# Kernel tuning notes

Hardware: AMD Instinct MI355X
Metric: run time of the kernel (lower is better)

The kernel has to match this reference:

```python
import jax, jax.numpy as jnp
import numpy as np

B, T, V = 8, 2048, 4096
BEAM = 8      # beam_size
BLANK = 0     # blank_id=0 in CTCBeamDecoder
TMP = 1.0     # temperature self.tmp


def setup_inputs() -> dict:
    key = jax.random.key(0)
    k1, k2 = jax.random.split(key)
    logits = jax.random.normal(k1, (B, T, V), dtype=jnp.float32)
    # valid frame counts in [T//2, T]
    lengths = jax.random.randint(k2, (B,), T // 2, T + 1).astype(jnp.int32)
    return {"logits": logits, "lengths": lengths}


def _beam_search_single(logP, length):
    """CTC beam search over alignments (no LM) for one utterance.
    logP: [T, V] log-probs, length: scalar valid frame count.
    Returns (collapsed_tokens [T] padded with -1, out_len, best_score).
    """
    scores0, toks0 = jax.lax.top_k(logP[0], BEAM)              # [BEAM]
    toks0 = toks0.astype(jnp.int32)
    bp0 = jnp.zeros((BEAM,), jnp.int32)

    def step(scores, xs):
        t, logp_t = xs
        cand = scores[:, None] + logp_t[None, :]               # [BEAM, V]
        new_scores, flat_idx = jax.lax.top_k(cand.reshape(-1), BEAM)
        bp = (flat_idx // V).astype(jnp.int32)
        tok = (flat_idx % V).astype(jnp.int32)
        valid = t < length
        new_scores = jnp.where(valid, new_scores, scores)
        bp = jnp.where(valid, bp, jnp.arange(BEAM, dtype=jnp.int32))
        tok = jnp.where(valid, tok, jnp.full((BEAM,), BLANK, jnp.int32))
        return new_scores, (tok, bp)

    ts = jnp.arange(1, T)
    final_scores, (toks, bps) = jax.lax.scan(step, scores0, (ts, logP[1:]))
    toks = jnp.concatenate([toks0[None], toks], axis=0)        # [T, BEAM]
    bps = jnp.concatenate([bp0[None], bps], axis=0)            # [T, BEAM]

    # backtrace best beam (index 0 after final top_k)
    def back(beam, xs):
        tok_t, bp_t = xs
        return bp_t[beam], tok_t[beam]
    _, path = jax.lax.scan(back, jnp.int32(0), (toks, bps), reverse=True)  # [T] in time order

    # CTC collapse: drop blanks and consecutive repeats, restrict to valid frames
    tpos = jnp.arange(T)
    prev = jnp.concatenate([jnp.array([-1], jnp.int32), path[:-1]])
    keep = (path != BLANK) & (path != prev) & (tpos < length)
    out_len = keep.sum().astype(jnp.int32)
    pos = jnp.cumsum(keep) - 1                                  # target slot for kept tokens
    idx = jnp.where(keep, pos, T)                               # dump non-kept into slot T
    out = jnp.full((T + 1,), -1, jnp.int32).at[idx].set(jnp.where(keep, path, -1))
    return out[:T], out_len, final_scores[0]


def reference(logits, lengths):
    # logits/tmp then log_softmax (the tensorized part of the torch module)
    logP = jax.nn.log_softmax(logits / TMP, axis=-1)            # [B, T, V]
    tokens, out_lens, best_scores = jax.vmap(_beam_search_single)(logP, lengths)
    return tokens, out_lens, best_scores, logP
```

## Files before the change

kernel.cpp:

```cpp
#include <hip/hip_runtime.h>
#include <cmath>

#define NB 8
#define NT 2048
#define NV 4096
#define NK 12

__device__ __forceinline__ void lds_fence() {
  asm volatile("s_waitcnt lgkmcnt(0)" ::: "memory");
}

__global__ __launch_bounds__(64, 4) void lsm_top12_kernel(
    const float* __restrict__ logits,
    float* __restrict__ out_logP,
    float* __restrict__ topPf,
    int* __restrict__ topI)
{
  const int row  = blockIdx.x;
  const int lane = threadIdx.x;
  const float4* __restrict__ x4 = (const float4*)(logits + (size_t)row * NV);

  float4 r[16];
  #pragma unroll
  for (int k = 0; k < 16; ++k) r[k] = x4[lane + (k << 6)];

  float m = -INFINITY;
  #pragma unroll
  for (int k = 0; k < 16; ++k)
    m = fmaxf(m, fmaxf(fmaxf(r[k].x, r[k].y), fmaxf(r[k].z, r[k].w)));
  #pragma unroll
  for (int off = 32; off > 0; off >>= 1) m = fmaxf(m, __shfl_xor(m, off, 64));

  float a0 = 0.0f, a1 = 0.0f, a2 = 0.0f, a3 = 0.0f;
  #pragma unroll
  for (int k = 0; k < 16; ++k) {
    a0 += __expf(r[k].x - m);
    a1 += __expf(r[k].y - m);
    a2 += __expf(r[k].z - m);
    a3 += __expf(r[k].w - m);
  }
  float accf = (a0 + a1) + (a2 + a3);
  #pragma unroll
  for (int off = 32; off > 0; off >>= 1) accf += __shfl_xor(accf, off, 64);
  const float L32 = logf(accf);

  float lv[NK]; int li[NK];
  #pragma unroll
  for (int z = 0; z < NK; ++z) { lv[z] = -INFINITY; li[z] = 0x7FFFFFFF; }

#define INS(VAL, IDX)                                                       \
  do {                                                                      \
    float _v = (VAL); int _i = (IDX);                                       \
    if (_v > lv[NK - 1]) {                                                  \
      lv[NK - 1] = _v; li[NK - 1] = _i;                                     \
      for (int z = NK - 1; z > 0; --z)                                      \
        if (lv[z] > lv[z - 1]) {                                            \
          float tv = lv[z]; lv[z] = lv[z - 1]; lv[z - 1] = tv;              \
          int   ti = li[z]; li[z] = li[z - 1]; li[z - 1] = ti;              \
        }                                                                   \
    }                                                                       \
  } while (0)

  float4* __restrict__ orow4 = (float4*)(out_logP + (size_t)row * NV);
  #pragma unroll
  for (int k = 0; k < 16; ++k) {
    const int vb = (lane + (k << 6)) << 2;
    float4 o;
    o.x = (r[k].x - m) - L32;
    o.y = (r[k].y - m) - L32;
    o.z = (r[k].z - m) - L32;
    o.w = (r[k].w - m) - L32;
    orow4[lane + (k << 6)] = o;
    const float g4 = fmaxf(fmaxf(o.x, o.y), fmaxf(o.z, o.w));
    if (g4 > lv[NK - 1]) {
      INS(o.x, vb); INS(o.y, vb + 1); INS(o.z, vb + 2); INS(o.w, vb + 3);
    }
  }
#undef INS

  float mv = 0.0f; int mi = 0;
  #pragma unroll
  for (int rr = 0; rr < NK; ++rr) {
    float cv = lv[0]; int ci = li[0];
    #pragma unroll
    for (int off = 32; off > 0; off >>= 1) {
      float ov = __shfl_xor(cv, off, 64);
      int   oi = __shfl_xor(ci, off, 64);
      if (ov > cv || (ov == cv && oi < ci)) { cv = ov; ci = oi; }
    }
    if (rr == 0)    { mv = cv; mi = ci; }
    if (lane == rr) { mv = cv; mi = ci; }
    if (lv[0] == cv && li[0] == ci) {
      for (int z = 0; z < NK - 1; ++z) { lv[z] = lv[z + 1]; li[z] = li[z + 1]; }
      lv[NK - 1] = -INFINITY; li[NK - 1] = 0x7FFFFFFF;
    }
  }
  if (lane < NK) {
    topPf[(size_t)row * NK + lane] = mv;
    topI [(size_t)row * NK + lane] = mi;
  }
}


#define LOADROW(P, V, R)                                                      \
  do {                                                                        \
    const int _r = (R) < NT ? (R) : (NT - 1);                                 \
    P = Pb[(size_t)_r * NK + j_l];                                            \
    V = Ib[(size_t)_r * NK + j_l];                                            \
  } while (0)

#define STEP(T, PV, VV)                                                       \
  do {                                                                        \
    const float cand = s + (PV);              \
    const unsigned int cb = ~__float_as_uint(cand);                           \
    const unsigned int flat = (unsigned int)((i_l << 12) | (VV));             \
    const unsigned long long key =                                            \
        ((unsigned long long)cb << 15) | (unsigned long long)(0x7FFFu ^ flat);\
    const unsigned int klo = (unsigned int)key;                               \
    const unsigned int khi = (unsigned int)(key >> 32);                       \
    int rank = 0;                                                             \
    _Pragma("unroll")                                                         \
    for (int mm = 0; mm < 31; ++mm) {                                         \
      const unsigned int olo =                                                \
          (unsigned int)__builtin_amdgcn_readlane((int)klo, mm);              \
      const unsigned int ohi =                                                \
          (unsigned int)__builtin_amdgcn_readlane((int)khi, mm);              \
      const unsigned long long ok = ((unsigned long long)ohi << 32) | olo;    \
      rank += (ok > key) ? 1 : 0;                                             \
    }                                                                         \
    const bool win = active && (rank < 8);                                    \
    const int sloti = win ? ((T) * 8 + rank) : (NT * 8 + lane);               \
    tokbp[sloti] = (unsigned short)(((VV) << 3) | i_l);                       \
    const int dst4 = win ? (rank << 2) : park4;                               \
    const int pushed =                                                        \
        __builtin_amdgcn_ds_permute(dst4, __float_as_int(cand));              \
    const float w0 = __uint_as_float((unsigned)__builtin_amdgcn_readlane(pushed, 0)); \
    const float w1 = __uint_as_float((unsigned)__builtin_amdgcn_readlane(pushed, 1)); \
    const float w2 = __uint_as_float((unsigned)__builtin_amdgcn_readlane(pushed, 2)); \
    const float w3 = __uint_as_float((unsigned)__builtin_amdgcn_readlane(pushed, 3)); \
    const float w4 = __uint_as_float((unsigned)__builtin_amdgcn_readlane(pushed, 4)); \
    const float w5 = __uint_as_float((unsigned)__builtin_amdgcn_readlane(pushed, 5)); \
    const float w6 = __uint_as_float((unsigned)__builtin_amdgcn_readlane(pushed, 6)); \
    const float w7 = __uint_as_float((unsigned)__builtin_amdgcn_readlane(pushed, 7)); \
    const float sA_ = b0 ? w1 : w0;                                           \
    const float sB_ = b0 ? w3 : w2;                                           \
    const float sC_ = b0 ? w5 : w4;                                           \
    const float sD_ = b0 ? w7 : w6;                                           \
    const float sE_ = b1 ? sB_ : sA_;                                         \
    const float sF_ = b1 ? sD_ : sC_;                                         \
    s = b2 ? sF_ : sE_;                                                       \
  } while (0)

__global__ __launch_bounds__(64) void beam_kernel(
    const float* __restrict__ topPf,
    const int* __restrict__ topI,
    const int* __restrict__ lengths,
    float* __restrict__ out_tok,
    float* __restrict__ out_lenA,
    float* __restrict__ out_scr)
{
  const int b    = blockIdx.x;
  const int lane = threadIdx.x;

  __shared__ unsigned short tokbp[NT * 8 + 64];
  __shared__ unsigned short pathA[NT];

  int len = lengths[b];
  if (len < 1) len = 1;
  if (len > NT) len = NT;

  int i_l = 0, j_l = 0; bool active = false;
  {
    int c = 0;
    #pragma unroll
    for (int i = 0; i < 8; ++i) {
      const int cnt = 12 / (i + 1);
      if (lane >= c && lane < c + cnt) { i_l = i; j_l = lane - c; active = true; }
      c += cnt;
    }
  }
  const bool b0 = (i_l & 1) != 0;
  const bool b1 = (i_l & 2) != 0;
  const bool b2 = (i_l & 4) != 0;
  const int  park4 = (32 + (lane & 31)) << 2;

  const float* __restrict__ Pb = topPf + (size_t)b * NT * NK;
  const int*   __restrict__ Ib = topI  + (size_t)b * NT * NK;

  {
    const float4* __restrict__ gp = (const float4*)Pb;
    const int4*   __restrict__ gi = (const int4*)Ib;
    float fa = 0.0f; int ia = 0;
    #pragma unroll 4
    for (int q = lane; q < NT * NK / 4; q += 64) {
      const float4 v = gp[q]; const int4 w = gi[q];
      fa += (v.x + v.y) + (v.z + v.w);
      ia ^= (w.x ^ w.y) ^ (w.z ^ w.w);
    }
    asm volatile("" :: "v"(fa), "v"(ia));
  }

  float s = Pb[i_l];
  if (lane < 8) tokbp[lane] = (unsigned short)(Ib[lane] << 3);

  float pA0, pA1, pA2, pA3, pB0, pB1, pB2, pB3;
  int   vA0, vA1, vA2, vA3, vB0, vB1, vB2, vB3;
  LOADROW(pA0, vA0, 1); LOADROW(pA1, vA1, 2);
  LOADROW(pA2, vA2, 3); LOADROW(pA3, vA3, 4);
  LOADROW(pB0, vB0, 5); LOADROW(pB1, vB1, 6);
  LOADROW(pB2, vB2, 7); LOADROW(pB3, vB3, 8);

  int t = 1;
  for (; t + 7 < len; t += 8) {
    STEP(t,     pA0, vA0);
    STEP(t + 1, pA1, vA1);
    STEP(t + 2, pA2, vA2);
    STEP(t + 3, pA3, vA3);
    LOADROW(pA0, vA0, t + 8);  LOADROW(pA1, vA1, t + 9);
    LOADROW(pA2, vA2, t + 10); LOADROW(pA3, vA3, t + 11);
    STEP(t + 4, pB0, vB0);
    STEP(t + 5, pB1, vB1);
    STEP(t + 6, pB2, vB2);
    STEP(t + 7, pB3, vB3);
    LOADROW(pB0, vB0, t + 12); LOADROW(pB1, vB1, t + 13);
    LOADROW(pB2, vB2, t + 14); LOADROW(pB3, vB3, t + 15);
  }
  if (t     < len) STEP(t,     pA0, vA0);
  if (t + 1 < len) STEP(t + 1, pA1, vA1);
  if (t + 2 < len) STEP(t + 2, pA2, vA2);
  if (t + 3 < len) STEP(t + 3, pA3, vA3);
  if (t + 4 < len) STEP(t + 4, pB0, vB0);
  if (t + 5 < len) STEP(t + 5, pB1, vB1);
  if (t + 6 < len) STEP(t + 6, pB2, vB2);

  lds_fence();
  if (lane == 0) {
    const uint4* __restrict__ rows = (const uint4*)tokbp;
#define EXT(R)                                                                \
    do {                                                                      \
      const unsigned long long half = (beam < 4)                              \
          ? (((unsigned long long)(R).y << 32) | (R).x)                       \
          : (((unsigned long long)(R).w << 32) | (R).z);                      \
      const int e = (int)((half >> ((beam & 3) << 4)) & 0xFFFFu);             \
      pathA[bt] = (unsigned short)(e >> 3);                                   \
      beam = e & 7;                                                           \
      --bt;                                                                   \
    } while (0)
    int beam = 0;
    int bt = len - 1;
    uint4 r0 = rows[bt];
    uint4 r1 = rows[bt >= 1 ? bt - 1 : 0];
    uint4 r2 = rows[bt >= 2 ? bt - 2 : 0];
    uint4 r3 = rows[bt >= 3 ? bt - 3 : 0];
    while (bt >= 7) {
      const uint4 n0 = rows[bt - 4], n1 = rows[bt - 5];
      const uint4 n2 = rows[bt - 6], n3 = rows[bt - 7];
      EXT(r0); EXT(r1); EXT(r2); EXT(r3);
      r0 = n0; r1 = n1; r2 = n2; r3 = n3;
    }
    while (bt >= 0) { const uint4 rr = rows[bt]; EXT(rr); }
#undef EXT
  }
  lds_fence();

  const int CH = NT / 64;
  const int base = lane * CH;
  int cnt = 0;
  for (int k = 0; k < CH; ++k) {
    int tt = base + k;
    if (tt < len) {
      int pt = pathA[tt];
      int pv = (tt > 0) ? (int)pathA[tt - 1] : -1;
      cnt += ((pt != 0) && (pt != pv)) ? 1 : 0;
    }
  }
  int incl = cnt;
  #pragma unroll
  for (int off = 1; off < 64; off <<= 1) {
    int n = __shfl_up(incl, off, 64);
    if (lane >= off) incl += n;
  }
  const int excl  = incl - cnt;
  const int total = __shfl(incl, 63, 64);

  float* __restrict__ ob = out_tok + (size_t)b * NT;
  int pos = excl;
  for (int k = 0; k < CH; ++k) {
    int tt = base + k;
    if (tt < len) {
      int pt = pathA[tt];
      int pv = (tt > 0) ? (int)pathA[tt - 1] : -1;
      if ((pt != 0) && (pt != pv)) { ob[pos] = (float)pt; ++pos; }
    }
  }
  for (int q = total + lane; q < NT; q += 64) ob[q] = -1.0f;

  if (lane == 0) {
    out_lenA[b] = (float)total;
    out_scr[b]  = s;
  }
}

#undef STEP
#undef LOADROW

extern "C" void kernel_launch(void* const* d_in, const int* in_sizes, int n_in,
                              void* d_out, int out_size, void* d_ws, size_t ws_size,
                              hipStream_t stream) {
  (void)in_sizes; (void)n_in; (void)out_size; (void)ws_size;
  const float* logits  = (const float*)d_in[0];
  const int*   lengths = (const int*)d_in[1];

  float* out_tok  = (float*)d_out;
  float* out_lenp = out_tok + NB * NT;
  float* out_scr  = out_lenp + NB;
  float* out_logP = out_scr + NB;

  float* topPf = (float*)d_ws;
  int*   topI  = (int*)(topPf + (size_t)NB * NT * NK);

  lsm_top12_kernel<<<NB * NT, 64, 0, stream>>>(logits, out_logP, topPf, topI);
  beam_kernel<<<NB, 64, 0, stream>>>(topPf, topI, lengths, out_tok, out_lenp, out_scr);
}
```

Measured before the change: 1.334 ms.

## Stream logsoftmax in chunks, split rank compare chains, drop cache prewarm

```diff
diff --git a/kernel.cpp b/kernel.cpp
--- a/kernel.cpp
+++ b/kernel.cpp
@@ -10,7 +10,7 @@
   asm volatile("s_waitcnt lgkmcnt(0)" ::: "memory");
 }
 
-__global__ __launch_bounds__(64, 4) void lsm_top12_kernel(
+__global__ __launch_bounds__(64, 6) void lsm_top12_kernel(
     const float* __restrict__ logits,
     float* __restrict__ out_logP,
     float* __restrict__ topPf,
@@ -20,26 +20,39 @@
   const int lane = threadIdx.x;
   const float4* __restrict__ x4 = (const float4*)(logits + (size_t)row * NV);
 
-  float4 r[16];
-  #pragma unroll
-  for (int k = 0; k < 16; ++k) r[k] = x4[lane + (k << 6)];
-
   float m = -INFINITY;
-  #pragma unroll
-  for (int k = 0; k < 16; ++k)
-    m = fmaxf(m, fmaxf(fmaxf(r[k].x, r[k].y), fmaxf(r[k].z, r[k].w)));
-  #pragma unroll
-  for (int off = 32; off > 0; off >>= 1) m = fmaxf(m, __shfl_xor(m, off, 64));
-
   float a0 = 0.0f, a1 = 0.0f, a2 = 0.0f, a3 = 0.0f;
-  #pragma unroll
-  for (int k = 0; k < 16; ++k) {
-    a0 += __expf(r[k].x - m);
-    a1 += __expf(r[k].y - m);
-    a2 += __expf(r[k].z - m);
-    a3 += __expf(r[k].w - m);
-  }
-  float accf = (a0 + a1) + (a2 + a3);
+  float4 f0 = x4[lane], f1 = x4[lane + 64], f2 = x4[lane + 128],
+         f3 = x4[lane + 192];
+  #pragma unroll
+  for (int c = 0; c < 4; ++c) {
+    float4 g0, g1, g2, g3;
+    if (c < 3) {
+      const int kb = lane + ((c + 1) << 8);
+      g0 = x4[kb]; g1 = x4[kb + 64]; g2 = x4[kb + 128]; g3 = x4[kb + 192];
+    } else { g0 = f0; g1 = f1; g2 = f2; g3 = f3; }
+    float cm = fmaxf(fmaxf(fmaxf(f0.x, f0.y), fmaxf(f0.z, f0.w)),
+                     fmaxf(fmaxf(f1.x, f1.y), fmaxf(f1.z, f1.w)));
+    cm = fmaxf(cm, fmaxf(fmaxf(fmaxf(f2.x, f2.y), fmaxf(f2.z, f2.w)),
+                         fmaxf(fmaxf(f3.x, f3.y), fmaxf(f3.z, f3.w))));
+    const float nm = fmaxf(m, cm);
+    const float sc = __expf(m - nm);
+    a0 = a0 * sc + (__expf(f0.x - nm) + __expf(f1.x - nm) +
+                    __expf(f2.x - nm) + __expf(f3.x - nm));
+    a1 = a1 * sc + (__expf(f0.y - nm) + __expf(f1.y - nm) +
+                    __expf(f2.y - nm) + __expf(f3.y - nm));
+    a2 = a2 * sc + (__expf(f0.z - nm) + __expf(f1.z - nm) +
+                    __expf(f2.z - nm) + __expf(f3.z - nm));
+    a3 = a3 * sc + (__expf(f0.w - nm) + __expf(f1.w - nm) +
+                    __expf(f2.w - nm) + __expf(f3.w - nm));
+    m = nm;
+    f0 = g0; f1 = g1; f2 = g2; f3 = g3;
+  }
+
+  float M = m;
+  #pragma unroll
+  for (int off = 32; off > 0; off >>= 1) M = fmaxf(M, __shfl_xor(M, off, 64));
+  float accf = ((a0 + a1) + (a2 + a3)) * __expf(m - M);
   #pragma unroll
   for (int off = 32; off > 0; off >>= 1) accf += __shfl_xor(accf, off, 64);
   const float L32 = logf(accf);
@@ -61,21 +74,36 @@
     }                                                                       \
   } while (0)
 
+#define DO4(F, KK)                                                          \
+  do {                                                                      \
+    const int idx = lane + ((KK) << 6);                                     \
+    const int vb  = idx << 2;                                               \
+    float4 o;                                                               \
+    o.x = (F.x - M) - L32;                                                  \
+    o.y = (F.y - M) - L32;                                                  \
+    o.z = (F.z - M) - L32;                                                  \
+    o.w = (F.w - M) - L32;                                                  \
+    orow4[idx] = o;                                                         \
+    const float g4 = fmaxf(fmaxf(o.x, o.y), fmaxf(o.z, o.w));               \
+    if (g4 > lv[NK - 1]) {         \
+      INS(o.x, vb); INS(o.y, vb + 1); INS(o.z, vb + 2); INS(o.w, vb + 3);   \
+    }                                                                       \
+  } while (0)
+
   float4* __restrict__ orow4 = (float4*)(out_logP + (size_t)row * NV);
-  #pragma unroll
-  for (int k = 0; k < 16; ++k) {
-    const int vb = (lane + (k << 6)) << 2;
-    float4 o;
-    o.x = (r[k].x - m) - L32;
-    o.y = (r[k].y - m) - L32;
-    o.z = (r[k].z - m) - L32;
-    o.w = (r[k].w - m) - L32;
-    orow4[lane + (k << 6)] = o;
-    const float g4 = fmaxf(fmaxf(o.x, o.y), fmaxf(o.z, o.w));
-    if (g4 > lv[NK - 1]) {
-      INS(o.x, vb); INS(o.y, vb + 1); INS(o.z, vb + 2); INS(o.w, vb + 3);
-    }
-  }
+  f0 = x4[lane]; f1 = x4[lane + 64]; f2 = x4[lane + 128]; f3 = x4[lane + 192];
+  #pragma unroll
+  for (int c = 0; c < 4; ++c) {
+    float4 g0, g1, g2, g3;
+    if (c < 3) {
+      const int kb = lane + ((c + 1) << 8);
+      g0 = x4[kb]; g1 = x4[kb + 64]; g2 = x4[kb + 128]; g3 = x4[kb + 192];
+    } else { g0 = f0; g1 = f1; g2 = f2; g3 = f3; }
+    DO4(f0, c * 4 + 0); DO4(f1, c * 4 + 1);
+    DO4(f2, c * 4 + 2); DO4(f3, c * 4 + 3);
+    f0 = g0; f1 = g1; f2 = g2; f3 = g3;
+  }
+#undef DO4
 #undef INS
 
   float mv = 0.0f; int mi = 0;
@@ -107,6 +135,22 @@
     const int _r = (R) < NT ? (R) : (NT - 1);                                 \
     P = Pb[(size_t)_r * NK + j_l];                                            \
     V = Ib[(size_t)_r * NK + j_l];                                            \
+  } while (0)
+
+#define CMP4(BASE, A0, A1, A2, A3)                                            \
+  do {                                                                        \
+    const unsigned int lo0 = (unsigned int)__builtin_amdgcn_readlane((int)klo, (BASE));     \
+    const unsigned int hi0 = (unsigned int)__builtin_amdgcn_readlane((int)khi, (BASE));     \
+    const unsigned int lo1 = (unsigned int)__builtin_amdgcn_readlane((int)klo, (BASE) + 1); \
+    const unsigned int hi1 = (unsigned int)__builtin_amdgcn_readlane((int)khi, (BASE) + 1); \
+    const unsigned int lo2 = (unsigned int)__builtin_amdgcn_readlane((int)klo, (BASE) + 2); \
+    const unsigned int hi2 = (unsigned int)__builtin_amdgcn_readlane((int)khi, (BASE) + 2); \
+    const unsigned int lo3 = (unsigned int)__builtin_amdgcn_readlane((int)klo, (BASE) + 3); \
+    const unsigned int hi3 = (unsigned int)__builtin_amdgcn_readlane((int)khi, (BASE) + 3); \
+    A0 += ((((unsigned long long)hi0 << 32) | lo0) > key) ? 1 : 0;            \
+    A1 += ((((unsigned long long)hi1 << 32) | lo1) > key) ? 1 : 0;            \
+    A2 += ((((unsigned long long)hi2 << 32) | lo2) > key) ? 1 : 0;            \
+    A3 += ((((unsigned long long)hi3 << 32) | lo3) > key) ? 1 : 0;            \
   } while (0)
 
 #define STEP(T, PV, VV)                                                       \
@@ -118,16 +162,26 @@
         ((unsigned long long)cb << 15) | (unsigned long long)(0x7FFFu ^ flat);\
     const unsigned int klo = (unsigned int)key;                               \
     const unsigned int khi = (unsigned int)(key >> 32);                       \
-    int rank = 0;                                                             \
-    _Pragma("unroll")                                                         \
-    for (int mm = 0; mm < 31; ++mm) {                                         \
-      const unsigned int olo =                                                \
-          (unsigned int)__builtin_amdgcn_readlane((int)klo, mm);              \
-      const unsigned int ohi =                                                \
-          (unsigned int)__builtin_amdgcn_readlane((int)khi, mm);              \
-      const unsigned long long ok = ((unsigned long long)ohi << 32) | olo;    \
-      rank += (ok > key) ? 1 : 0;                                             \
+    int r0_ = 0, r1_ = 0, r2_ = 0, r3_ = 0;                                   \
+    CMP4(0,  r0_, r1_, r2_, r3_);                                             \
+    CMP4(4,  r0_, r1_, r2_, r3_);                                             \
+    CMP4(8,  r0_, r1_, r2_, r3_);                                             \
+    CMP4(12, r0_, r1_, r2_, r3_);                                             \
+    CMP4(16, r0_, r1_, r2_, r3_);                                             \
+    CMP4(20, r0_, r1_, r2_, r3_);                                             \
+    CMP4(24, r0_, r1_, r2_, r3_);                                             \
+    {                                                                         \
+      const unsigned int lo0 = (unsigned int)__builtin_amdgcn_readlane((int)klo, 28); \
+      const unsigned int hi0 = (unsigned int)__builtin_amdgcn_readlane((int)khi, 28); \
+      const unsigned int lo1 = (unsigned int)__builtin_amdgcn_readlane((int)klo, 29); \
+      const unsigned int hi1 = (unsigned int)__builtin_amdgcn_readlane((int)khi, 29); \
+      const unsigned int lo2 = (unsigned int)__builtin_amdgcn_readlane((int)klo, 30); \
+      const unsigned int hi2 = (unsigned int)__builtin_amdgcn_readlane((int)khi, 30); \
+      r0_ += ((((unsigned long long)hi0 << 32) | lo0) > key) ? 1 : 0;         \
+      r1_ += ((((unsigned long long)hi1 << 32) | lo1) > key) ? 1 : 0;         \
+      r2_ += ((((unsigned long long)hi2 << 32) | lo2) > key) ? 1 : 0;         \
     }                                                                         \
+    const int rank = (r0_ + r1_) + (r2_ + r3_);                               \
     const bool win = active && (rank < 8);                                    \
     const int sloti = win ? ((T) * 8 + rank) : (NT * 8 + lane);               \
     tokbp[sloti] = (unsigned short)(((VV) << 3) | i_l);                       \
@@ -186,19 +240,6 @@
 
   const float* __restrict__ Pb = topPf + (size_t)b * NT * NK;
   const int*   __restrict__ Ib = topI  + (size_t)b * NT * NK;
-
-  {
-    const float4* __restrict__ gp = (const float4*)Pb;
-    const int4*   __restrict__ gi = (const int4*)Ib;
-    float fa = 0.0f; int ia = 0;
-    #pragma unroll 4
-    for (int q = lane; q < NT * NK / 4; q += 64) {
-      const float4 v = gp[q]; const int4 w = gi[q];
-      fa += (v.x + v.y) + (v.z + v.w);
-      ia ^= (w.x ^ w.y) ^ (w.z ^ w.w);
-    }
-    asm volatile("" :: "v"(fa), "v"(ia));
-  }
 
   float s = Pb[i_l];
   if (lane < 8) tokbp[lane] = (unsigned short)(Ib[lane] << 3);
@@ -302,6 +343,7 @@
 }
 
 #undef STEP
+#undef CMP4
 #undef LOADROW
 
 extern "C" void kernel_launch(void* const* d_in, const int* in_sizes, int n_in,
```

Result: slower. 1.461 ms (+9.5%).
